# Kernel tuning notes

Measured on AMD Instinct MI355X. Metric: run time of the kernel, lower is better.

Reference implementation:

```python
import jax, jax.numpy as jnp
import numpy as np

N = 100000      # nodes
E = 1600000     # edges (avg degree 16)
IN, HID, OUT = 128, 32, 16
H = 2           # attention heads
EPS = 1e-5
NEG_SLOPE = 0.2


def setup_inputs() -> dict:
    key = jax.random.key(0)
    ks = jax.random.split(key, 24)
    f32 = jnp.float32
    def w(k, shape, scale=0.1):
        return jax.random.normal(k, shape, f32) * scale
    return {
        "x": jax.random.normal(ks[0], (N, IN), f32),
        "edge_index": jax.random.randint(ks[1], (2, E), 0, N, dtype=jnp.int32),
        # GCN layer 1
        "gcn1_W": w(ks[2], (IN, HID)), "gcn1_b": w(ks[3], (HID,)),
        # BN1 (eval mode: running stats)
        "bn1_g": 1.0 + w(ks[4], (HID,)), "bn1_b": w(ks[5], (HID,)),
        "bn1_m": w(ks[6], (HID,)), "bn1_v": 1.0 + jnp.abs(w(ks[7], (HID,))),
        # GAT layer 1 (HID -> HID, heads=H, concat=False)
        "gat1_W": w(ks[8], (HID, H * HID)), "gat1_as": w(ks[9], (H, HID)),
        "gat1_ad": w(ks[10], (H, HID)), "gat1_b": w(ks[11], (HID,)),
        # GCN layer 2
        "gcn2_W": w(ks[12], (HID, HID)), "gcn2_b": w(ks[13], (HID,)),
        # BN2
        "bn2_g": 1.0 + w(ks[14], (HID,)), "bn2_b": w(ks[15], (HID,)),
        "bn2_m": w(ks[16], (HID,)), "bn2_v": 1.0 + jnp.abs(w(ks[17], (HID,))),
        # GAT layer 2 (HID -> OUT, heads=H, concat=False)
        "gat2_W": w(ks[18], (HID, H * OUT)), "gat2_as": w(ks[19], (H, OUT)),
        "gat2_ad": w(ks[20], (H, OUT)), "gat2_b": w(ks[21], (OUT,)),
    }


def _add_self_loops(edge_index):
    loop = jnp.arange(N, dtype=edge_index.dtype)
    src = jnp.concatenate([edge_index[0], loop])
    dst = jnp.concatenate([edge_index[1], loop])
    return src, dst


def _gcn(x, src, dst, W, b):
    h = x @ W                                             # [N, F]
    deg = jax.ops.segment_sum(jnp.ones_like(dst, h.dtype), dst, N)
    dinv = jax.lax.rsqrt(jnp.maximum(deg, 1.0))
    norm = dinv[src] * dinv[dst]                          # [Etot]
    out = jax.ops.segment_sum(h[src] * norm[:, None], dst, N)
    return out + b


def _gat(x, src, dst, W, a_src, a_dst, b, F):
    # PyG GATConv (concat=False -> mean over heads); eval mode (no attn dropout)
    h = (x @ W).reshape(N, H, F)                          # [N, H, F]
    al_s = jnp.einsum('nhf,hf->nh', h, a_src)             # [N, H]
    al_d = jnp.einsum('nhf,hf->nh', h, a_dst)
    e = jax.nn.leaky_relu(al_s[src] + al_d[dst], NEG_SLOPE)  # [Etot, H]
    # segment softmax over destination neighborhoods (self-loops ensure >=1 edge)
    m = jax.ops.segment_max(e, dst, N)
    ex = jnp.exp(e - m[dst])
    s = jax.ops.segment_sum(ex, dst, N)
    alpha = ex / s[dst]                                   # [Etot, H]
    out = jax.ops.segment_sum(alpha[:, :, None] * h[src], dst, N)  # [N, H, F]
    return out.mean(axis=1) + b


def _bn_eval(x, g, b, m, v):
    return (x - m) * jax.lax.rsqrt(v + EPS) * g + b


def reference(x, edge_index, gcn1_W, gcn1_b, bn1_g, bn1_b, bn1_m, bn1_v,
              gat1_W, gat1_as, gat1_ad, gat1_b, gcn2_W, gcn2_b,
              bn2_g, bn2_b, bn2_m, bn2_v, gat2_W, gat2_as, gat2_ad, gat2_b):
    src, dst = _add_self_loops(edge_index)
    h = _gcn(x, src, dst, gcn1_W, gcn1_b)
    h = jax.nn.relu(_bn_eval(h, bn1_g, bn1_b, bn1_m, bn1_v))
    h = jax.nn.relu(_gat(h, src, dst, gat1_W, gat1_as, gat1_ad, gat1_b, HID))
    h = _gcn(h, src, dst, gcn2_W, gcn2_b)
    h = jax.nn.relu(_bn_eval(h, bn2_g, bn2_b, bn2_m, bn2_v))
    h = _gat(h, src, dst, gat2_W, gat2_as, gat2_ad, gat2_b, OUT)
    return jax.nn.log_softmax(h, axis=1)
```

## Files before the change

### kernel.cpp

```cpp
#include <hip/hip_runtime.h>
#include <hip/hip_bf16.h>

#define NN 100000
#define EE 1600000
#define SLAB 64
#define KB 391
#define CHUNK 4096
#define BSLAB 4736

static constexpr float EPSV = 1e-5f;
static constexpr float SLOPE = 0.2f;

__device__ __forceinline__ float lrelu(float v) { return v > 0.f ? v : SLOPE * v; }

__device__ __forceinline__ unsigned rne_bf16(float v) {
    unsigned u = __float_as_uint(v);
    return (u + 0x7fffu + ((u >> 16) & 1u)) >> 16;
}
__device__ __forceinline__ float bf16_lo(unsigned u) { return __uint_as_float(u << 16); }
__device__ __forceinline__ float bf16_hi(unsigned u) { return __uint_as_float(u & 0xffff0000u); }


__global__ void k_z(int* __restrict__ bcnt, unsigned* __restrict__ hsp,
                    unsigned* __restrict__ g1p, unsigned* __restrict__ g2p) {
    int i = threadIdx.x;
    if (i < KB) bcnt[i] = 0;
    if (i < 16) hsp[(size_t)NN * 16 + i] = 0u;
    if (i < 32) g1p[(size_t)NN * 32 + i] = 0u;
    if (i < 16) g2p[(size_t)NN * 16 + i] = 0u;
}

__global__ __launch_bounds__(256) void k_scat(const int* __restrict__ src, const int* __restrict__ dst,
                                              int* __restrict__ bcnt, unsigned int* __restrict__ ebuf) {
    __shared__ int hc[KB], hb[KB];
    int tid = threadIdx.x;
    for (int i = tid; i < KB; i += 256) hc[i] = 0;
    __syncthreads();
    int e0 = blockIdx.x * CHUNK;
    #pragma unroll
    for (int r = 0; r < CHUNK / 256; ++r) {
        int e = e0 + r * 256 + tid;
        if (e < EE) atomicAdd(&hc[dst[e] >> 8], 1);
    }
    __syncthreads();
    for (int i = tid; i < KB; i += 256) {
        int c = hc[i];
        if (c) hb[i] = atomicAdd(&bcnt[i], c);
        hc[i] = 0;
    }
    __syncthreads();
    #pragma unroll
    for (int r = 0; r < CHUNK / 256; ++r) {
        int e = e0 + r * 256 + tid;
        if (e < EE) {
            int d = dst[e];
            int b = d >> 8;
            int rk = atomicAdd(&hc[b], 1);
            ebuf[(size_t)b * BSLAB + hb[b] + rk] = ((unsigned)src[e] << 8) | (unsigned)(d & 255);
        }
    }
}

__global__ __launch_bounds__(256) void k_bucket(const unsigned int* __restrict__ ebuf,
                                                const int* __restrict__ bcnt,
                                                int* __restrict__ col, int* __restrict__ cnt,
                                                float* __restrict__ dinv) {
    __shared__ int lc[256];
    int tid = threadIdx.x;
    int b = blockIdx.x;
    lc[tid] = 0;
    __syncthreads();
    size_t s = (size_t)b * BSLAB;
    int nb = bcnt[b];
    for (int i = tid; i < nb; i += 256) {
        unsigned v = ebuf[s + i];
        int l = v & 255;
        int r = atomicAdd(&lc[l], 1);
        col[(((b << 8) + l) << 6) + r] = v >> 8;
    }
    __syncthreads();
    int node = (b << 8) + tid;
    if (node < NN) {
        int c = lc[tid];
        cnt[node] = c;
        dinv[node] = rsqrtf((float)(c + 1));
        col[node * SLAB + c] = node;
        for (int j = c + 1; j < 32; ++j) col[node * SLAB + j] = NN;
    }
}


__global__ __launch_bounds__(256) void k_gemm1(const float* __restrict__ x,
                                               const float* __restrict__ W,
                                               const float* __restrict__ dinv,
                                               unsigned* __restrict__ hsp) {
    __shared__ float xs[64][128];
    int tid = threadIdx.x;
    int lane = tid & 63;
    int wv = tid >> 6;
    int khalf = lane >> 5, f = lane & 31;
    float wreg[64];
    const float* wp = W + (khalf * 64) * 32 + f;
    #pragma unroll
    for (int i = 0; i < 64; ++i) wreg[i] = wp[i * 32];
    int n0 = blockIdx.x * 64;
    for (int i = tid; i < 64 * 32; i += 256) {
        int row = i >> 5, c4 = i & 31;
        int n = n0 + row;
        float4 v = (n < NN) ? *(const float4*)&x[(size_t)n * 128 + c4 * 4]
                            : make_float4(0.f, 0.f, 0.f, 0.f);
        *(float4*)&xs[row][c4 * 4] = v;
    }
    __syncthreads();
    #pragma unroll 4
    for (int t = 0; t < 16; ++t) {
        int row = wv * 16 + t;
        int n = n0 + row;
        if (n >= NN) break;
        const float* xp = &xs[row][khalf * 64];
        float a0 = 0.f, a1 = 0.f, a2 = 0.f, a3 = 0.f;
        #pragma unroll
        for (int j = 0; j < 16; j += 4) {
            float4 v0 = *(const float4*)&xp[(j + 0) * 4];
            float4 v1 = *(const float4*)&xp[(j + 1) * 4];
            float4 v2 = *(const float4*)&xp[(j + 2) * 4];
            float4 v3 = *(const float4*)&xp[(j + 3) * 4];
            a0 += v0.x * wreg[j * 4 + 0]  + v0.y * wreg[j * 4 + 1]  + v0.z * wreg[j * 4 + 2]  + v0.w * wreg[j * 4 + 3];
            a1 += v1.x * wreg[j * 4 + 4]  + v1.y * wreg[j * 4 + 5]  + v1.z * wreg[j * 4 + 6]  + v1.w * wreg[j * 4 + 7];
            a2 += v2.x * wreg[j * 4 + 8]  + v2.y * wreg[j * 4 + 9]  + v2.z * wreg[j * 4 + 10] + v2.w * wreg[j * 4 + 11];
            a3 += v3.x * wreg[j * 4 + 12] + v3.y * wreg[j * 4 + 13] + v3.z * wreg[j * 4 + 14] + v3.w * wreg[j * 4 + 15];
        }
        float tot = (a0 + a1) + (a2 + a3);
        tot += __shfl_xor(tot, 32);
        unsigned r16 = rne_bf16(tot * dinv[n]);
        unsigned hi16 = __shfl(r16, f + 1, 32);
        if (khalf == 0 && !(f & 1))
            hsp[n * 16 + (f >> 1)] = (hi16 << 16) | (r16 & 0xffffu);
    }
}

__device__ __forceinline__ float quad_reduce_u2(const uint2* u, int lane) {
    float ac0 = 0.f, ac1 = 0.f, ac2 = 0.f, ac3 = 0.f;
    #pragma unroll
    for (int s = 0; s < 8; ++s) {
        ac0 += bf16_lo(u[s].x); ac1 += bf16_hi(u[s].x);
        ac2 += bf16_lo(u[s].y); ac3 += bf16_hi(u[s].y);
    }
    ac0 += __shfl_xor(ac0, 8); ac0 += __shfl_xor(ac0, 16);
    ac1 += __shfl_xor(ac1, 8); ac1 += __shfl_xor(ac1, 16);
    ac2 += __shfl_xor(ac2, 8); ac2 += __shfl_xor(ac2, 16);
    ac3 += __shfl_xor(ac3, 8); ac3 += __shfl_xor(ac3, 16);
    int p = lane >> 2;
    float v0 = __shfl(ac0, p, 32), v1 = __shfl(ac1, p, 32);
    float v2 = __shfl(ac2, p, 32), v3 = __shfl(ac3, p, 32);
    float s01 = (lane & 1) ? v1 : v0;
    float s23 = (lane & 1) ? v3 : v2;
    return (lane & 2) ? s23 : s01;
}

__device__ __forceinline__ float gen_sum_hsp(const unsigned* hsp, const int* col, int base,
                                             int dn, int lane) {
    int half = lane >> 4, l16 = lane & 15;
    int c0 = col[base + lane];
    int c1 = col[base + 32 + lane];
    float aL0 = 0.f, aH0 = 0.f, aL1 = 0.f, aH1 = 0.f;
    for (int j2 = 0; j2 < dn; j2 += 4) {
        int eA = j2 + half, eB = j2 + 2 + half;
        int cA = __shfl((j2 < 32) ? c0 : c1, eA & 31, 32);
        int cB = __shfl((j2 + 2 < 32) ? c0 : c1, eB & 31, 32);
        bool okA = eA < dn, okB = eB < dn;
        unsigned uA = hsp[(okA ? cA : 0) * 16 + l16];
        unsigned uB = hsp[(okB ? cB : 0) * 16 + l16];
        uA = okA ? uA : 0u; uB = okB ? uB : 0u;
        aL0 += bf16_lo(uA); aH0 += bf16_hi(uA);
        aL1 += bf16_lo(uB); aH1 += bf16_hi(uB);
    }
    float accLo = aL0 + aL1, accHi = aH0 + aH1;
    accLo += __shfl_xor(accLo, 16);
    accHi += __shfl_xor(accHi, 16);
    float vLo = __shfl(accLo, lane >> 1, 32);
    float vHi = __shfl(accHi, lane >> 1, 32);
    return (lane & 1) ? vHi : vLo;
}


__global__ __launch_bounds__(256) void k_gcn1_gat1t(
    const unsigned* __restrict__ hsp, const int* __restrict__ cnt,
    const int* __restrict__ col, const float* __restrict__ dinv,
    const float* __restrict__ gb, const float* __restrict__ bng,
    const float* __restrict__ bnb, const float* __restrict__ bnm,
    const float* __restrict__ bnv,
    const float* __restrict__ W1, const float* __restrict__ as_, const float* __restrict__ ad_,
    unsigned* __restrict__ gp, float* __restrict__ al) {
    __shared__ float wAs[32][32], wBs[32][32];
    int tid = threadIdx.x;
    int r = tid >> 5, lane = tid & 31;
    int n = blockIdx.x * 8 + r;
    int dn = cnt[n] + 1;
    int base = n * SLAB;
    int c0 = col[base + lane];
    bool common = (dn <= 32);
    uint2 u[8];
    if (common) {
        int q = lane & 7, sub = lane >> 3;
        const uint2* h2 = (const uint2*)hsp;
        #pragma unroll
        for (int s = 0; s < 8; ++s) {
            int c = __shfl(c0, 4 * s + sub, 32);
            u[s] = h2[(size_t)c * 8 + q];
        }
    }
    for (int i = tid; i < 1024; i += 256) {
        int k = i >> 5, f = i & 31;
        wAs[k][f] = W1[k * 64 + f];
        wBs[k][f] = W1[k * 64 + 32 + f];
    }
    __syncthreads();
    float acc;
    if (common) acc = quad_reduce_u2(u, lane);
    else        acc = gen_sum_hsp(hsp, col, base, dn, lane);
    float v = dinv[n] * acc + gb[lane];
    v = (v - bnm[lane]) * rsqrtf(bnv[lane] + EPSV) * bng[lane] + bnb[lane];
    v = fmaxf(v, 0.f);
    float gA0 = 0.f, gA1 = 0.f, gB0 = 0.f, gB1 = 0.f;
    #pragma unroll
    for (int k = 0; k < 32; k += 2) {
        float t0 = __shfl(v, k, 32);
        float t1v = __shfl(v, k + 1, 32);
        gA0 += t0 * wAs[k][lane];     gB0 += t0 * wBs[k][lane];
        gA1 += t1v * wAs[k + 1][lane]; gB1 += t1v * wBs[k + 1][lane];
    }
    float gA = gA0 + gA1, gB = gB0 + gB1;
    float pas0 = gA * as_[lane],      pad0 = gA * ad_[lane];
    float pas1 = gB * as_[32 + lane], pad1 = gB * ad_[32 + lane];
    #pragma unroll
    for (int off = 16; off; off >>= 1) {
        pas0 += __shfl_xor(pas0, off);
        pad0 += __shfl_xor(pad0, off);
        pas1 += __shfl_xor(pas1, off);
        pad1 += __shfl_xor(pad1, off);
    }
    if (lane == 0) *(float4*)&al[n * 4] = make_float4(pas0, pas1, pad0, pad1);
    gp[n * 32 + lane] = (rne_bf16(gB) << 16) | rne_bf16(gA);
}


__global__ __launch_bounds__(256) void k_gat1_pv(
    const unsigned* __restrict__ gp, const float* __restrict__ al,
    const int* __restrict__ cnt, const int* __restrict__ col,
    const float* __restrict__ b, const float* __restrict__ W2,
    const float* __restrict__ dinv, unsigned* __restrict__ hs3p) {
    __shared__ float2 ec[8][SLAB];
    __shared__ float w2s[32][32];
    int tid = threadIdx.x;
    int r = tid >> 5, lane = tid & 31;
    int n = blockIdx.x * 8 + r;
    int dn = cnt[n] + 1;
    int base = n * SLAB;
    int c0 = col[base + lane];
    int c1 = (dn > 32) ? col[base + 32 + lane] : (int)NN;
    bool common = (dn <= 32);
    uint4 u[8];
    if (common) {
        int q = lane & 7, sub = lane >> 3;
        const uint4* g4 = (const uint4*)gp;
        #pragma unroll
        for (int s = 0; s < 8; ++s) {
            int c = __shfl(c0, 4 * s + sub, 32);
            u[s] = g4[(size_t)c * 8 + q];
        }
    }
    for (int i = tid; i < 1024; i += 256) w2s[i >> 5][i & 31] = W2[i];
    float ad0 = al[n * 4 + 2], ad1 = al[n * 4 + 3];
    float e0a = -1e30f, e1a = -1e30f, e0b = -1e30f, e1b = -1e30f;
    if (lane < dn) {
        float4 a4 = *(const float4*)&al[(size_t)c0 * 4];
        e0a = lrelu(a4.x + ad0); e1a = lrelu(a4.y + ad1);
    }
    if (32 + lane < dn) {
        float4 a4 = *(const float4*)&al[(size_t)c1 * 4];
        e0b = lrelu(a4.x + ad0); e1b = lrelu(a4.y + ad1);
    }
    float m0 = fmaxf(e0a, e0b), m1 = fmaxf(e1a, e1b);
    #pragma unroll
    for (int off = 16; off; off >>= 1) {
        m0 = fmaxf(m0, __shfl_xor(m0, off));
        m1 = fmaxf(m1, __shfl_xor(m1, off));
    }
    float x0a = (lane < dn) ? __expf(e0a - m0) : 0.f;
    float x1a = (lane < dn) ? __expf(e1a - m1) : 0.f;
    float x0b = (32 + lane < dn) ? __expf(e0b - m0) : 0.f;
    float x1b = (32 + lane < dn) ? __expf(e1b - m1) : 0.f;
    float s0 = x0a + x0b, s1 = x1a + x1b;
    #pragma unroll
    for (int off = 16; off; off >>= 1) {
        s0 += __shfl_xor(s0, off);
        s1 += __shfl_xor(s1, off);
    }
    float A0, A1;
    if (common) {
        int sub = lane >> 3;
        float aL0 = 0.f, aL1 = 0.f, aL2 = 0.f, aL3 = 0.f;
        float aH0 = 0.f, aH1 = 0.f, aH2 = 0.f, aH3 = 0.f;
        #pragma unroll
        for (int s = 0; s < 8; ++s) {
            int e = 4 * s + sub;
            float w0 = __shfl(x0a, e, 32);
            float w1 = __shfl(x1a, e, 32);
            aL0 += w0 * bf16_lo(u[s].x); aH0 += w1 * bf16_hi(u[s].x);
            aL1 += w0 * bf16_lo(u[s].y); aH1 += w1 * bf16_hi(u[s].y);
            aL2 += w0 * bf16_lo(u[s].z); aH2 += w1 * bf16_hi(u[s].z);
            aL3 += w0 * bf16_lo(u[s].w); aH3 += w1 * bf16_hi(u[s].w);
        }
        aL0 += __shfl_xor(aL0, 8); aL0 += __shfl_xor(aL0, 16);
        aL1 += __shfl_xor(aL1, 8); aL1 += __shfl_xor(aL1, 16);
        aL2 += __shfl_xor(aL2, 8); aL2 += __shfl_xor(aL2, 16);
        aL3 += __shfl_xor(aL3, 8); aL3 += __shfl_xor(aL3, 16);
        aH0 += __shfl_xor(aH0, 8); aH0 += __shfl_xor(aH0, 16);
        aH1 += __shfl_xor(aH1, 8); aH1 += __shfl_xor(aH1, 16);
        aH2 += __shfl_xor(aH2, 8); aH2 += __shfl_xor(aH2, 16);
        aH3 += __shfl_xor(aH3, 8); aH3 += __shfl_xor(aH3, 16);
        int p = lane >> 2;
        float l0 = __shfl(aL0, p, 32), l1 = __shfl(aL1, p, 32);
        float l2 = __shfl(aL2, p, 32), l3 = __shfl(aL3, p, 32);
        float h0 = __shfl(aH0, p, 32), h1 = __shfl(aH1, p, 32);
        float h2 = __shfl(aH2, p, 32), h3 = __shfl(aH3, p, 32);
        float sl01 = (lane & 1) ? l1 : l0, sl23 = (lane & 1) ? l3 : l2;
        float sh01 = (lane & 1) ? h1 : h0, sh23 = (lane & 1) ? h3 : h2;
        A0 = (lane & 2) ? sl23 : sl01;
        A1 = (lane & 2) ? sh23 : sh01;
    } else {
        ec[r][lane] = make_float2(x0a, x1a);
        ec[r][32 + lane] = make_float2(x0b, x1b);
        int half = lane >> 4, l16 = lane & 15;
        const uint2* gp2 = (const uint2*)gp;
        float a0L = 0.f, a0H = 0.f, a1L = 0.f, a1H = 0.f;
        float b0L = 0.f, b0H = 0.f, b1L = 0.f, b1H = 0.f;
        for (int j2 = 0; j2 < dn; j2 += 4) {
            int eA = j2 + half, eB = j2 + 2 + half;
            int cA = __shfl((j2 < 32) ? c0 : c1, eA & 31, 32);
            int cB = __shfl((j2 + 2 < 32) ? c0 : c1, eB & 31, 32);
            bool okA = eA < dn, okB = eB < dn;
            uint2 uA = gp2[(size_t)(okA ? cA : 0) * 16 + l16];
            uint2 uB = gp2[(size_t)(okB ? cB : 0) * 16 + l16];
            float2 wA = ec[r][eA & 63];
            float2 wB = ec[r][eB & 63];
            uA.x = okA ? uA.x : 0u; uA.y = okA ? uA.y : 0u;
            uB.x = okB ? uB.x : 0u; uB.y = okB ? uB.y : 0u;
            a0L += wA.x * bf16_lo(uA.x); a1L += wA.y * bf16_hi(uA.x);
            a0H += wA.x * bf16_lo(uA.y); a1H += wA.y * bf16_hi(uA.y);
            b0L += wB.x * bf16_lo(uB.x); b1L += wB.y * bf16_hi(uB.x);
            b0H += wB.x * bf16_lo(uB.y); b1H += wB.y * bf16_hi(uB.y);
        }
        a0L += b0L; a0H += b0H; a1L += b1L; a1H += b1H;
        a0L += __shfl_xor(a0L, 16); a0H += __shfl_xor(a0H, 16);
        a1L += __shfl_xor(a1L, 16); a1H += __shfl_xor(a1H, 16);
        int p = lane >> 1;
        float t0L = __shfl(a0L, p, 32), t0H = __shfl(a0H, p, 32);
        float t1L = __shfl(a1L, p, 32), t1H = __shfl(a1H, p, 32);
        A0 = (lane & 1) ? t0H : t0L;
        A1 = (lane & 1) ? t1H : t1L;
    }
    __syncthreads();
    float v = 0.5f * (A0 / s0 + A1 / s1) + b[lane];
    v = fmaxf(v, 0.f);
    float g0 = 0.f, g1 = 0.f;
    #pragma unroll
    for (int k = 0; k < 32; k += 2) {
        g0 += __shfl(v, k, 32) * w2s[k][lane];
        g1 += __shfl(v, k + 1, 32) * w2s[k + 1][lane];
    }
    unsigned r16 = rne_bf16((g0 + g1) * dinv[n]);
    unsigned hi16 = __shfl(r16, lane + 1, 32);
    if (!(lane & 1)) hs3p[n * 16 + (lane >> 1)] = (hi16 << 16) | (r16 & 0xffffu);
}


__global__ __launch_bounds__(256) void k_gcn2_gat2t(
    const unsigned* __restrict__ hsp, const int* __restrict__ cnt,
    const int* __restrict__ col, const float* __restrict__ dinv,
    const float* __restrict__ gb, const float* __restrict__ bng,
    const float* __restrict__ bnb, const float* __restrict__ bnm,
    const float* __restrict__ bnv,
    const float* __restrict__ Wg, const float* __restrict__ as_, const float* __restrict__ ad_,
    unsigned* __restrict__ g2p, float* __restrict__ al) {
    __shared__ float wgs[32][32];
    int tid = threadIdx.x;
    int r = tid >> 5, lane = tid & 31;
    int n = blockIdx.x * 8 + r;
    int dn = cnt[n] + 1;
    int base = n * SLAB;
    int c0 = col[base + lane];
    bool common = (dn <= 32);
    uint2 u[8];
    if (common) {
        int q = lane & 7, sub = lane >> 3;
        const uint2* h2 = (const uint2*)hsp;
        #pragma unroll
        for (int s = 0; s < 8; ++s) {
            int c = __shfl(c0, 4 * s + sub, 32);
            u[s] = h2[(size_t)c * 8 + q];
        }
    }
    for (int i = tid; i < 1024; i += 256) wgs[i >> 5][i & 31] = Wg[i];
    __syncthreads();
    float acc;
    if (common) acc = quad_reduce_u2(u, lane);
    else        acc = gen_sum_hsp(hsp, col, base, dn, lane);
    float v = dinv[n] * acc + gb[lane];
    v = (v - bnm[lane]) * rsqrtf(bnv[lane] + EPSV) * bng[lane] + bnb[lane];
    v = fmaxf(v, 0.f);
    float g0 = 0.f, g1 = 0.f;
    #pragma unroll
    for (int k = 0; k < 32; k += 2) {
        g0 += __shfl(v, k, 32) * wgs[k][lane];
        g1 += __shfl(v, k + 1, 32) * wgs[k + 1][lane];
    }
    float g = g0 + g1;
    int hh = lane >> 4, ff = lane & 15;
    float as_v = g * as_[hh * 16 + ff];
    float ad_v = g * ad_[hh * 16 + ff];
    #pragma unroll
    for (int off = 8; off; off >>= 1) {
        as_v += __shfl_xor(as_v, off);
        ad_v += __shfl_xor(ad_v, off);
    }
    if (ff == 0) { al[n * 4 + hh] = as_v; al[n * 4 + 2 + hh] = ad_v; }
    unsigned r16 = rne_bf16(g);
    unsigned hi16 = __shfl(r16, lane + 1, 32);
    if (!(lane & 1)) g2p[n * 16 + (lane >> 1)] = (hi16 << 16) | (r16 & 0xffffu);
}


__global__ __launch_bounds__(256) void k_gat2_agg(
    const unsigned* __restrict__ g2p, const float* __restrict__ al,
    const int* __restrict__ cnt, const int* __restrict__ col,
    const float* __restrict__ b, float* __restrict__ out) {
    __shared__ float2 ec[8][SLAB];
    int tid = threadIdx.x;
    int r = tid >> 5, lane = tid & 31;
    int n = blockIdx.x * 8 + r;
    int dn = cnt[n] + 1;
    int base = n * SLAB;
    int c0 = col[base + lane];
    int c1 = (dn > 32) ? col[base + 32 + lane] : (int)NN;
    bool common = (dn <= 32);
    uint2 u[8];
    if (common) {
        int q = lane & 7, sub = lane >> 3;
        const uint2* g2 = (const uint2*)g2p;
        #pragma unroll
        for (int s = 0; s < 8; ++s) {
            int c = __shfl(c0, 4 * s + sub, 32);
            u[s] = g2[(size_t)c * 8 + q];
        }
    }
    float ad0 = al[n * 4 + 2], ad1 = al[n * 4 + 3];
    float e0a = -1e30f, e1a = -1e30f, e0b = -1e30f, e1b = -1e30f;
    if (lane < dn) {
        float4 a4 = *(const float4*)&al[(size_t)c0 * 4];
        e0a = lrelu(a4.x + ad0); e1a = lrelu(a4.y + ad1);
    }
    if (32 + lane < dn) {
        float4 a4 = *(const float4*)&al[(size_t)c1 * 4];
        e0b = lrelu(a4.x + ad0); e1b = lrelu(a4.y + ad1);
    }
    float m0 = fmaxf(e0a, e0b), m1 = fmaxf(e1a, e1b);
    #pragma unroll
    for (int off = 16; off; off >>= 1) {
        m0 = fmaxf(m0, __shfl_xor(m0, off));
        m1 = fmaxf(m1, __shfl_xor(m1, off));
    }
    float x0a = (lane < dn) ? __expf(e0a - m0) : 0.f;
    float x1a = (lane < dn) ? __expf(e1a - m1) : 0.f;
    float x0b = (32 + lane < dn) ? __expf(e0b - m0) : 0.f;
    float x1b = (32 + lane < dn) ? __expf(e1b - m1) : 0.f;
    float s0 = x0a + x0b, s1 = x1a + x1b;
    #pragma unroll
    for (int off = 16; off; off >>= 1) {
        s0 += __shfl_xor(s0, off);
        s1 += __shfl_xor(s1, off);
    }
    float acc;
    if (common) {
        int sub = lane >> 3;
        bool head1 = (lane & 4) != 0;
        float ac0 = 0.f, ac1 = 0.f, ac2 = 0.f, ac3 = 0.f;
        #pragma unroll
        for (int s = 0; s < 8; ++s) {
            int e = 4 * s + sub;
            float w0 = __shfl(x0a, e, 32);
            float w1 = __shfl(x1a, e, 32);
            float w = head1 ? w1 : w0;
            ac0 += w * bf16_lo(u[s].x); ac1 += w * bf16_hi(u[s].x);
            ac2 += w * bf16_lo(u[s].y); ac3 += w * bf16_hi(u[s].y);
        }
        ac0 += __shfl_xor(ac0, 8); ac0 += __shfl_xor(ac0, 16);
        ac1 += __shfl_xor(ac1, 8); ac1 += __shfl_xor(ac1, 16);
        ac2 += __shfl_xor(ac2, 8); ac2 += __shfl_xor(ac2, 16);
        ac3 += __shfl_xor(ac3, 8); ac3 += __shfl_xor(ac3, 16);
        int p = lane >> 2;
        float v0 = __shfl(ac0, p, 32), v1 = __shfl(ac1, p, 32);
        float v2 = __shfl(ac2, p, 32), v3 = __shfl(ac3, p, 32);
        float s01 = (lane & 1) ? v1 : v0;
        float s23 = (lane & 1) ? v3 : v2;
        acc = (lane & 2) ? s23 : s01;
    } else {
        ec[r][lane] = make_float2(x0a, x1a);
        ec[r][32 + lane] = make_float2(x0b, x1b);
        int half = lane >> 4, l16 = lane & 15;
        bool head1g = (l16 & 8) != 0;
        float aL0 = 0.f, aH0 = 0.f, aL1 = 0.f, aH1 = 0.f;
        for (int j2 = 0; j2 < dn; j2 += 4) {
            int eA = j2 + half, eB = j2 + 2 + half;
            int cA = __shfl((j2 < 32) ? c0 : c1, eA & 31, 32);
            int cB = __shfl((j2 + 2 < 32) ? c0 : c1, eB & 31, 32);
            bool okA = eA < dn, okB = eB < dn;
            unsigned uA = g2p[(okA ? cA : 0) * 16 + l16];
            unsigned uB = g2p[(okB ? cB : 0) * 16 + l16];
            float2 wA = ec[r][eA & 63];
            float2 wB = ec[r][eB & 63];
            float wa = head1g ? wA.y : wA.x;
            float wb = head1g ? wB.y : wB.x;
            uA = okA ? uA : 0u; uB = okB ? uB : 0u;
            aL0 += wa * bf16_lo(uA); aH0 += wa * bf16_hi(uA);
            aL1 += wb * bf16_lo(uB); aH1 += wb * bf16_hi(uB);
        }
        float accLo = aL0 + aL1, accHi = aH0 + aH1;
        accLo += __shfl_xor(accLo, 16);
        accHi += __shfl_xor(accHi, 16);
        float vLo = __shfl(accLo, lane >> 1, 32);
        float vHi = __shfl(accHi, lane >> 1, 32);
        acc = (lane & 1) ? vHi : vLo;
    }
    int hh = lane >> 4, ff = lane & 15;
    acc /= (hh ? s1 : s0);
    float v = 0.5f * (acc + __shfl_xor(acc, 16)) + b[ff];
    float mx = v;
    #pragma unroll
    for (int off = 8; off; off >>= 1) mx = fmaxf(mx, __shfl_xor(mx, off));
    float se = __expf(v - mx);
    #pragma unroll
    for (int off = 8; off; off >>= 1) se += __shfl_xor(se, off);
    if (hh == 0) out[(size_t)n * 16 + ff] = v - mx - __logf(se);
}


static inline size_t al256(size_t x) { return (x + 255) & ~((size_t)255); }

extern "C" void kernel_launch(void* const* d_in, const int* in_sizes, int n_in,
                              void* d_out, int out_size, void* d_ws, size_t ws_size,
                              hipStream_t stream) {
    const float* x      = (const float*)d_in[0];
    const int*   ei     = (const int*)d_in[1];
    const float* gcn1_W = (const float*)d_in[2];
    const float* gcn1_b = (const float*)d_in[3];
    const float* bn1_g  = (const float*)d_in[4];
    const float* bn1_b  = (const float*)d_in[5];
    const float* bn1_m  = (const float*)d_in[6];
    const float* bn1_v  = (const float*)d_in[7];
    const float* gat1_W = (const float*)d_in[8];
    const float* gat1_as= (const float*)d_in[9];
    const float* gat1_ad= (const float*)d_in[10];
    const float* gat1_b = (const float*)d_in[11];
    const float* gcn2_W = (const float*)d_in[12];
    const float* gcn2_b = (const float*)d_in[13];
    const float* bn2_g  = (const float*)d_in[14];
    const float* bn2_b  = (const float*)d_in[15];
    const float* bn2_m  = (const float*)d_in[16];
    const float* bn2_v  = (const float*)d_in[17];
    const float* gat2_W = (const float*)d_in[18];
    const float* gat2_as= (const float*)d_in[19];
    const float* gat2_ad= (const float*)d_in[20];
    const float* gat2_b = (const float*)d_in[21];
    float* out = (float*)d_out;

    char* w = (char*)d_ws;
    size_t off = 0;
    auto alloc = [&](size_t bytes) { void* p = w + off; off = al256(off + bytes); return p; };
    int*      cnt   = (int*)alloc((size_t)NN * 4);
    float*    dinv  = (float*)alloc((size_t)NN * 4);
    int*      col   = (int*)alloc((size_t)NN * SLAB * 4);
    unsigned* hsp   = (unsigned*)alloc((size_t)(NN + 1) * 16 * 4);
    unsigned* g1p   = (unsigned*)alloc((size_t)(NN + 1) * 32 * 4);
    unsigned* g2p   = (unsigned*)alloc((size_t)(NN + 1) * 16 * 4);
    float*    al    = (float*)alloc((size_t)NN * 4 * 4);
    int*      bcnt  = (int*)alloc((size_t)KB * 4);
    unsigned int* ebuf = (unsigned int*)g1p;

    const int* esrc = ei;
    const int* edst = ei + EE;
    const int GE = (EE + CHUNK - 1) / CHUNK;

    k_z<<<1, 512, 0, stream>>>(bcnt, hsp, g1p, g2p);
    k_scat<<<GE, 256, 0, stream>>>(esrc, edst, bcnt, ebuf);
    k_bucket<<<KB, 256, 0, stream>>>(ebuf, bcnt, col, cnt, dinv);

    k_gemm1<<<(NN + 63) / 64, 256, 0, stream>>>(x, gcn1_W, dinv, hsp);
    k_gcn1_gat1t<<<NN / 8, 256, 0, stream>>>(hsp, cnt, col, dinv, gcn1_b,
                                             bn1_g, bn1_b, bn1_m, bn1_v,
                                             gat1_W, gat1_as, gat1_ad, g1p, al);
    k_gat1_pv<<<NN / 8, 256, 0, stream>>>(g1p, al, cnt, col, gat1_b,
                                          gcn2_W, dinv, hsp);
    k_gcn2_gat2t<<<NN / 8, 256, 0, stream>>>(hsp, cnt, col, dinv, gcn2_b,
                                             bn2_g, bn2_b, bn2_m, bn2_v,
                                             gat2_W, gat2_as, gat2_ad, g2p, al);
    k_gat2_agg<<<NN / 8, 256, 0, stream>>>(g2p, al, cnt, col, gat2_b, out);
}
```

Measured before the change: 287.9 us.

## Drop max-subtraction in GAT softmax, fuse exp into gather, split attention logits

Removes the segment-max pass and its cross-lane reductions from both GAT aggregation kernels. Each lane now computes exp(lrelu(as+ad)) inline while gathering neighbour features and accumulates the denominator alongside the numerator, which also drops the shared-memory weight buffer. Attention logits are split into separate source and destination float2 arrays, and a sentinel row at index NN (zero features, -1e30 logits) replaces the per-edge predicated loads. This trades a dependent max/exp pre-pass for more exp work per gathered element. Without max subtraction, exp can overflow for large logits.

After: 265.4 us. 1.08x faster.

```diff
diff --git a/kernel.cpp b/kernel.cpp
--- a/kernel.cpp
+++ b/kernel.cpp
@@ -22,12 +22,14 @@
 
 
 __global__ void k_z(int* __restrict__ bcnt, unsigned* __restrict__ hsp,
-                    unsigned* __restrict__ g1p, unsigned* __restrict__ g2p) {
+                    unsigned* __restrict__ g1p, unsigned* __restrict__ g2p,
+                    float2* __restrict__ als) {
     int i = threadIdx.x;
     if (i < KB) bcnt[i] = 0;
     if (i < 16) hsp[(size_t)NN * 16 + i] = 0u;
     if (i < 32) g1p[(size_t)NN * 32 + i] = 0u;
     if (i < 16) g2p[(size_t)NN * 16 + i] = 0u;
+    if (i == 0) als[NN] = make_float2(-1e30f, -1e30f);
 }
 
 __global__ __launch_bounds__(256) void k_scat(const int* __restrict__ src, const int* __restrict__ dst,
@@ -168,10 +170,10 @@
         int eA = j2 + half, eB = j2 + 2 + half;
         int cA = __shfl((j2 < 32) ? c0 : c1, eA & 31, 32);
         int cB = __shfl((j2 + 2 < 32) ? c0 : c1, eB & 31, 32);
-        bool okA = eA < dn, okB = eB < dn;
-        unsigned uA = hsp[(okA ? cA : 0) * 16 + l16];
-        unsigned uB = hsp[(okB ? cB : 0) * 16 + l16];
-        uA = okA ? uA : 0u; uB = okB ? uB : 0u;
+        cA = (eA < dn) ? cA : (int)NN;
+        cB = (eB < dn) ? cB : (int)NN;
+        unsigned uA = hsp[(size_t)cA * 16 + l16];
+        unsigned uB = hsp[(size_t)cB * 16 + l16];
         aL0 += bf16_lo(uA); aH0 += bf16_hi(uA);
         aL1 += bf16_lo(uB); aH1 += bf16_hi(uB);
     }
@@ -191,7 +193,7 @@
     const float* __restrict__ bnb, const float* __restrict__ bnm,
     const float* __restrict__ bnv,
     const float* __restrict__ W1, const float* __restrict__ as_, const float* __restrict__ ad_,
-    unsigned* __restrict__ gp, float* __restrict__ al) {
+    unsigned* __restrict__ gp, float2* __restrict__ als, float2* __restrict__ ald) {
     __shared__ float wAs[32][32], wBs[32][32];
     int tid = threadIdx.x;
     int r = tid >> 5, lane = tid & 31;
@@ -240,17 +242,17 @@
         pas1 += __shfl_xor(pas1, off);
         pad1 += __shfl_xor(pad1, off);
     }
-    if (lane == 0) *(float4*)&al[n * 4] = make_float4(pas0, pas1, pad0, pad1);
+    if (lane == 0) { als[n] = make_float2(pas0, pas1); ald[n] = make_float2(pad0, pad1); }
     gp[n * 32 + lane] = (rne_bf16(gB) << 16) | rne_bf16(gA);
 }
 
 
 __global__ __launch_bounds__(256) void k_gat1_pv(
-    const unsigned* __restrict__ gp, const float* __restrict__ al,
+    const unsigned* __restrict__ gp, const float2* __restrict__ als,
+    const float2* __restrict__ ald,
     const int* __restrict__ cnt, const int* __restrict__ col,
     const float* __restrict__ b, const float* __restrict__ W2,
     const float* __restrict__ dinv, unsigned* __restrict__ hs3p) {
-    __shared__ float2 ec[8][SLAB];
     __shared__ float w2s[32][32];
     int tid = threadIdx.x;
     int r = tid >> 5, lane = tid & 31;
@@ -258,59 +260,27 @@
     int dn = cnt[n] + 1;
     int base = n * SLAB;
     int c0 = col[base + lane];
-    int c1 = (dn > 32) ? col[base + 32 + lane] : (int)NN;
-    bool common = (dn <= 32);
-    uint4 u[8];
-    if (common) {
+    float2 ad = ald[n];
+    for (int i = tid; i < 1024; i += 256) w2s[i >> 5][i & 31] = W2[i];
+    float A0, A1, ws0, ws1;
+    if (dn <= 32) {
         int q = lane & 7, sub = lane >> 3;
         const uint4* g4 = (const uint4*)gp;
+        float aL0 = 0.f, aL1 = 0.f, aL2 = 0.f, aL3 = 0.f;
+        float aH0 = 0.f, aH1 = 0.f, aH2 = 0.f, aH3 = 0.f;
+        float w0s = 0.f, w1s = 0.f;
         #pragma unroll
         for (int s = 0; s < 8; ++s) {
             int c = __shfl(c0, 4 * s + sub, 32);
-            u[s] = g4[(size_t)c * 8 + q];
-        }
-    }
-    for (int i = tid; i < 1024; i += 256) w2s[i >> 5][i & 31] = W2[i];
-    float ad0 = al[n * 4 + 2], ad1 = al[n * 4 + 3];
-    float e0a = -1e30f, e1a = -1e30f, e0b = -1e30f, e1b = -1e30f;
-    if (lane < dn) {
-        float4 a4 = *(const float4*)&al[(size_t)c0 * 4];
-        e0a = lrelu(a4.x + ad0); e1a = lrelu(a4.y + ad1);
-    }
-    if (32 + lane < dn) {
-        float4 a4 = *(const float4*)&al[(size_t)c1 * 4];
-        e0b = lrelu(a4.x + ad0); e1b = lrelu(a4.y + ad1);
-    }
-    float m0 = fmaxf(e0a, e0b), m1 = fmaxf(e1a, e1b);
-    #pragma unroll
-    for (int off = 16; off; off >>= 1) {
-        m0 = fmaxf(m0, __shfl_xor(m0, off));
-        m1 = fmaxf(m1, __shfl_xor(m1, off));
-    }
-    float x0a = (lane < dn) ? __expf(e0a - m0) : 0.f;
-    float x1a = (lane < dn) ? __expf(e1a - m1) : 0.f;
-    float x0b = (32 + lane < dn) ? __expf(e0b - m0) : 0.f;
-    float x1b = (32 + lane < dn) ? __expf(e1b - m1) : 0.f;
-    float s0 = x0a + x0b, s1 = x1a + x1b;
-    #pragma unroll
-    for (int off = 16; off; off >>= 1) {
-        s0 += __shfl_xor(s0, off);
-        s1 += __shfl_xor(s1, off);
-    }
-    float A0, A1;
-    if (common) {
-        int sub = lane >> 3;
-        float aL0 = 0.f, aL1 = 0.f, aL2 = 0.f, aL3 = 0.f;
-        float aH0 = 0.f, aH1 = 0.f, aH2 = 0.f, aH3 = 0.f;
-        #pragma unroll
-        for (int s = 0; s < 8; ++s) {
-            int e = 4 * s + sub;
-            float w0 = __shfl(x0a, e, 32);
-            float w1 = __shfl(x1a, e, 32);
-            aL0 += w0 * bf16_lo(u[s].x); aH0 += w1 * bf16_hi(u[s].x);
-            aL1 += w0 * bf16_lo(u[s].y); aH1 += w1 * bf16_hi(u[s].y);
-            aL2 += w0 * bf16_lo(u[s].z); aH2 += w1 * bf16_hi(u[s].z);
-            aL3 += w0 * bf16_lo(u[s].w); aH3 += w1 * bf16_hi(u[s].w);
+            uint4 u = g4[(size_t)c * 8 + q];
+            float2 sl = als[c];
+            float w0 = __expf(lrelu(sl.x + ad.x));
+            float w1 = __expf(lrelu(sl.y + ad.y));
+            aL0 += w0 * bf16_lo(u.x); aH0 += w1 * bf16_hi(u.x);
+            aL1 += w0 * bf16_lo(u.y); aH1 += w1 * bf16_hi(u.y);
+            aL2 += w0 * bf16_lo(u.z); aH2 += w1 * bf16_hi(u.z);
+            aL3 += w0 * bf16_lo(u.w); aH3 += w1 * bf16_hi(u.w);
+            w0s += w0; w1s += w1;
         }
         aL0 += __shfl_xor(aL0, 8); aL0 += __shfl_xor(aL0, 16);
         aL1 += __shfl_xor(aL1, 8); aL1 += __shfl_xor(aL1, 16);
@@ -320,6 +290,8 @@
         aH1 += __shfl_xor(aH1, 8); aH1 += __shfl_xor(aH1, 16);
         aH2 += __shfl_xor(aH2, 8); aH2 += __shfl_xor(aH2, 16);
         aH3 += __shfl_xor(aH3, 8); aH3 += __shfl_xor(aH3, 16);
+        w0s += __shfl_xor(w0s, 8); w0s += __shfl_xor(w0s, 16);
+        w1s += __shfl_xor(w1s, 8); w1s += __shfl_xor(w1s, 16);
         int p = lane >> 2;
         float l0 = __shfl(aL0, p, 32), l1 = __shfl(aL1, p, 32);
         float l2 = __shfl(aL2, p, 32), l3 = __shfl(aL3, p, 32);
@@ -329,40 +301,42 @@
         float sh01 = (lane & 1) ? h1 : h0, sh23 = (lane & 1) ? h3 : h2;
         A0 = (lane & 2) ? sl23 : sl01;
         A1 = (lane & 2) ? sh23 : sh01;
+        ws0 = w0s; ws1 = w1s;
     } else {
-        ec[r][lane] = make_float2(x0a, x1a);
-        ec[r][32 + lane] = make_float2(x0b, x1b);
+        int c1 = col[base + 32 + lane];
         int half = lane >> 4, l16 = lane & 15;
         const uint2* gp2 = (const uint2*)gp;
         float a0L = 0.f, a0H = 0.f, a1L = 0.f, a1H = 0.f;
-        float b0L = 0.f, b0H = 0.f, b1L = 0.f, b1H = 0.f;
+        float w0s = 0.f, w1s = 0.f;
         for (int j2 = 0; j2 < dn; j2 += 4) {
             int eA = j2 + half, eB = j2 + 2 + half;
             int cA = __shfl((j2 < 32) ? c0 : c1, eA & 31, 32);
             int cB = __shfl((j2 + 2 < 32) ? c0 : c1, eB & 31, 32);
-            bool okA = eA < dn, okB = eB < dn;
-            uint2 uA = gp2[(size_t)(okA ? cA : 0) * 16 + l16];
-            uint2 uB = gp2[(size_t)(okB ? cB : 0) * 16 + l16];
-            float2 wA = ec[r][eA & 63];
-            float2 wB = ec[r][eB & 63];
-            uA.x = okA ? uA.x : 0u; uA.y = okA ? uA.y : 0u;
-            uB.x = okB ? uB.x : 0u; uB.y = okB ? uB.y : 0u;
-            a0L += wA.x * bf16_lo(uA.x); a1L += wA.y * bf16_hi(uA.x);
-            a0H += wA.x * bf16_lo(uA.y); a1H += wA.y * bf16_hi(uA.y);
-            b0L += wB.x * bf16_lo(uB.x); b1L += wB.y * bf16_hi(uB.x);
-            b0H += wB.x * bf16_lo(uB.y); b1H += wB.y * bf16_hi(uB.y);
-        }
-        a0L += b0L; a0H += b0H; a1L += b1L; a1H += b1H;
+            cA = (eA < dn) ? cA : (int)NN;
+            cB = (eB < dn) ? cB : (int)NN;
+            uint2 uA = gp2[(size_t)cA * 16 + l16];
+            uint2 uB = gp2[(size_t)cB * 16 + l16];
+            float2 sA = als[cA], sB = als[cB];
+            float wA0 = __expf(lrelu(sA.x + ad.x)), wA1 = __expf(lrelu(sA.y + ad.y));
+            float wB0 = __expf(lrelu(sB.x + ad.x)), wB1 = __expf(lrelu(sB.y + ad.y));
+            a0L += wA0 * bf16_lo(uA.x) + wB0 * bf16_lo(uB.x);
+            a1L += wA1 * bf16_hi(uA.x) + wB1 * bf16_hi(uB.x);
+            a0H += wA0 * bf16_lo(uA.y) + wB0 * bf16_lo(uB.y);
+            a1H += wA1 * bf16_hi(uA.y) + wB1 * bf16_hi(uB.y);
+            w0s += wA0 + wB0; w1s += wA1 + wB1;
+        }
         a0L += __shfl_xor(a0L, 16); a0H += __shfl_xor(a0H, 16);
         a1L += __shfl_xor(a1L, 16); a1H += __shfl_xor(a1H, 16);
+        w0s += __shfl_xor(w0s, 16); w1s += __shfl_xor(w1s, 16);
         int p = lane >> 1;
         float t0L = __shfl(a0L, p, 32), t0H = __shfl(a0H, p, 32);
         float t1L = __shfl(a1L, p, 32), t1H = __shfl(a1H, p, 32);
         A0 = (lane & 1) ? t0H : t0L;
         A1 = (lane & 1) ? t1H : t1L;
-    }
-    __syncthreads();
-    float v = 0.5f * (A0 / s0 + A1 / s1) + b[lane];
+        ws0 = w0s; ws1 = w1s;
+    }
+    __syncthreads();
+    float v = 0.5f * (A0 / ws0 + A1 / ws1) + b[lane];
     v = fmaxf(v, 0.f);
     float g0 = 0.f, g1 = 0.f;
     #pragma unroll
@@ -383,7 +357,7 @@
     const float* __restrict__ bnb, const float* __restrict__ bnm,
     const float* __restrict__ bnv,
     const float* __restrict__ Wg, const float* __restrict__ as_, const float* __restrict__ ad_,
-    unsigned* __restrict__ g2p, float* __restrict__ al) {
+    unsigned* __restrict__ g2p, float2* __restrict__ als, float2* __restrict__ ald) {
     __shared__ float wgs[32][32];
     int tid = threadIdx.x;
     int r = tid >> 5, lane = tid & 31;
@@ -425,7 +399,13 @@
         as_v += __shfl_xor(as_v, off);
         ad_v += __shfl_xor(ad_v, off);
     }
-    if (ff == 0) { al[n * 4 + hh] = as_v; al[n * 4 + 2 + hh] = ad_v; }
+    if (lane == 0) {
+        float s1v = __shfl(as_v, 16, 32);
+        float d1v = __shfl(ad_v, 16, 32);
+        als[n] = make_float2(as_v, s1v);
+        ald[n] = make_float2(ad_v, d1v);
+    } else if (lane == 16) {
+    }
     unsigned r16 = rne_bf16(g);
     unsigned hi16 = __shfl(r16, lane + 1, 32);
     if (!(lane & 1)) g2p[n * 16 + (lane >> 1)] = (hi16 << 16) | (r16 & 0xffffu);
@@ -433,108 +413,84 @@
 
 
 __global__ __launch_bounds__(256) void k_gat2_agg(
-    const unsigned* __restrict__ g2p, const float* __restrict__ al,
+    const unsigned* __restrict__ g2p, const float2* __restrict__ als,
+    const float2* __restrict__ ald,
     const int* __restrict__ cnt, const int* __restrict__ col,
     const float* __restrict__ b, float* __restrict__ out) {
-    __shared__ float2 ec[8][SLAB];
     int tid = threadIdx.x;
     int r = tid >> 5, lane = tid & 31;
     int n = blockIdx.x * 8 + r;
     int dn = cnt[n] + 1;
     int base = n * SLAB;
     int c0 = col[base + lane];
-    int c1 = (dn > 32) ? col[base + 32 + lane] : (int)NN;
-    bool common = (dn <= 32);
-    uint2 u[8];
-    if (common) {
+    float2 ad = ald[n];
+    float acc, ws0, ws1;
+    if (dn <= 32) {
         int q = lane & 7, sub = lane >> 3;
+        bool head1 = (lane & 4) != 0;
         const uint2* g2 = (const uint2*)g2p;
+        float ac0 = 0.f, ac1 = 0.f, ac2 = 0.f, ac3 = 0.f;
+        float w0s = 0.f, w1s = 0.f;
         #pragma unroll
         for (int s = 0; s < 8; ++s) {
             int c = __shfl(c0, 4 * s + sub, 32);
-            u[s] = g2[(size_t)c * 8 + q];
-        }
-    }
-    float ad0 = al[n * 4 + 2], ad1 = al[n * 4 + 3];
-    float e0a = -1e30f, e1a = -1e30f, e0b = -1e30f, e1b = -1e30f;
-    if (lane < dn) {
-        float4 a4 = *(const float4*)&al[(size_t)c0 * 4];
-        e0a = lrelu(a4.x + ad0); e1a = lrelu(a4.y + ad1);
-    }
-    if (32 + lane < dn) {
-        float4 a4 = *(const float4*)&al[(size_t)c1 * 4];
-        e0b = lrelu(a4.x + ad0); e1b = lrelu(a4.y + ad1);
-    }
-    float m0 = fmaxf(e0a, e0b), m1 = fmaxf(e1a, e1b);
-    #pragma unroll
-    for (int off = 16; off; off >>= 1) {
-        m0 = fmaxf(m0, __shfl_xor(m0, off));
-        m1 = fmaxf(m1, __shfl_xor(m1, off));
-    }
-    float x0a = (lane < dn) ? __expf(e0a - m0) : 0.f;
-    float x1a = (lane < dn) ? __expf(e1a - m1) : 0.f;
-    float x0b = (32 + lane < dn) ? __expf(e0b - m0) : 0.f;
-    float x1b = (32 + lane < dn) ? __expf(e1b - m1) : 0.f;
-    float s0 = x0a + x0b, s1 = x1a + x1b;
-    #pragma unroll
-    for (int off = 16; off; off >>= 1) {
-        s0 += __shfl_xor(s0, off);
-        s1 += __shfl_xor(s1, off);
-    }
-    float acc;
-    if (common) {
-        int sub = lane >> 3;
-        bool head1 = (lane & 4) != 0;
-        float ac0 = 0.f, ac1 = 0.f, ac2 = 0.f, ac3 = 0.f;
-        #pragma unroll
-        for (int s = 0; s < 8; ++s) {
-            int e = 4 * s + sub;
-            float w0 = __shfl(x0a, e, 32);
-            float w1 = __shfl(x1a, e, 32);
+            uint2 u = g2[(size_t)c * 8 + q];
+            float2 sl = als[c];
+            float w0 = __expf(lrelu(sl.x + ad.x));
+            float w1 = __expf(lrelu(sl.y + ad.y));
             float w = head1 ? w1 : w0;
-            ac0 += w * bf16_lo(u[s].x); ac1 += w * bf16_hi(u[s].x);
-            ac2 += w * bf16_lo(u[s].y); ac3 += w * bf16_hi(u[s].y);
+            ac0 += w * bf16_lo(u.x); ac1 += w * bf16_hi(u.x);
+            ac2 += w * bf16_lo(u.y); ac3 += w * bf16_hi(u.y);
+            w0s += w0; w1s += w1;
         }
         ac0 += __shfl_xor(ac0, 8); ac0 += __shfl_xor(ac0, 16);
         ac1 += __shfl_xor(ac1, 8); ac1 += __shfl_xor(ac1, 16);
         ac2 += __shfl_xor(ac2, 8); ac2 += __shfl_xor(ac2, 16);
         ac3 += __shfl_xor(ac3, 8); ac3 += __shfl_xor(ac3, 16);
+        w0s += __shfl_xor(w0s, 8); w0s += __shfl_xor(w0s, 16);
+        w1s += __shfl_xor(w1s, 8); w1s += __shfl_xor(w1s, 16);
         int p = lane >> 2;
         float v0 = __shfl(ac0, p, 32), v1 = __shfl(ac1, p, 32);
         float v2 = __shfl(ac2, p, 32), v3 = __shfl(ac3, p, 32);
         float s01 = (lane & 1) ? v1 : v0;
         float s23 = (lane & 1) ? v3 : v2;
         acc = (lane & 2) ? s23 : s01;
+        ws0 = w0s; ws1 = w1s;
     } else {
-        ec[r][lane] = make_float2(x0a, x1a);
-        ec[r][32 + lane] = make_float2(x0b, x1b);
+        int c1 = col[base + 32 + lane];
         int half = lane >> 4, l16 = lane & 15;
         bool head1g = (l16 & 8) != 0;
         float aL0 = 0.f, aH0 = 0.f, aL1 = 0.f, aH1 = 0.f;
+        float w0s = 0.f, w1s = 0.f;
         for (int j2 = 0; j2 < dn; j2 += 4) {
             int eA = j2 + half, eB = j2 + 2 + half;
             int cA = __shfl((j2 < 32) ? c0 : c1, eA & 31, 32);
             int cB = __shfl((j2 + 2 < 32) ? c0 : c1, eB & 31, 32);
-            bool okA = eA < dn, okB = eB < dn;
-            unsigned uA = g2p[(okA ? cA : 0) * 16 + l16];
-            unsigned uB = g2p[(okB ? cB : 0) * 16 + l16];
-            float2 wA = ec[r][eA & 63];
-            float2 wB = ec[r][eB & 63];
-            float wa = head1g ? wA.y : wA.x;
-            float wb = head1g ? wB.y : wB.x;
-            uA = okA ? uA : 0u; uB = okB ? uB : 0u;
+            cA = (eA < dn) ? cA : (int)NN;
+            cB = (eB < dn) ? cB : (int)NN;
+            unsigned uA = g2p[(size_t)cA * 16 + l16];
+            unsigned uB = g2p[(size_t)cB * 16 + l16];
+            float2 sA = als[cA], sB = als[cB];
+            float wA0 = __expf(lrelu(sA.x + ad.x)), wA1 = __expf(lrelu(sA.y + ad.y));
+            float wB0 = __expf(lrelu(sB.x + ad.x)), wB1 = __expf(lrelu(sB.y + ad.y));
+            float wa = head1g ? wA1 : wA0;
+            float wb = head1g ? wB1 : wB0;
             aL0 += wa * bf16_lo(uA); aH0 += wa * bf16_hi(uA);
             aL1 += wb * bf16_lo(uB); aH1 += wb * bf16_hi(uB);
+            w0s += wA0 + wB0; w1s += wA1 + wB1;
         }
         float accLo = aL0 + aL1, accHi = aH0 + aH1;
         accLo += __shfl_xor(accLo, 16);
         accHi += __shfl_xor(accHi, 16);
+        w0s += __shfl_xor(w0s, 16);
+        w1s += __shfl_xor(w1s, 16);
         float vLo = __shfl(accLo, lane >> 1, 32);
         float vHi = __shfl(accHi, lane >> 1, 32);
         acc = (lane & 1) ? vHi : vLo;
+        ws0 = w0s; ws1 = w1s;
     }
     int hh = lane >> 4, ff = lane & 15;
-    acc /= (hh ? s1 : s0);
+    acc /= (hh ? ws1 : ws0);
     float v = 0.5f * (acc + __shfl_xor(acc, 16)) + b[ff];
     float mx = v;
     #pragma unroll
@@ -584,7 +540,8 @@
     unsigned* hsp   = (unsigned*)alloc((size_t)(NN + 1) * 16 * 4);
     unsigned* g1p   = (unsigned*)alloc((size_t)(NN + 1) * 32 * 4);
     unsigned* g2p   = (unsigned*)alloc((size_t)(NN + 1) * 16 * 4);
-    float*    al    = (float*)alloc((size_t)NN * 4 * 4);
+    float2*   als   = (float2*)alloc((size_t)(NN + 1) * 8);
+    float2*   ald   = (float2*)alloc((size_t)NN * 8);
     int*      bcnt  = (int*)alloc((size_t)KB * 4);
     unsigned int* ebuf = (unsigned int*)g1p;
 
@@ -592,18 +549,18 @@
     const int* edst = ei + EE;
     const int GE = (EE + CHUNK - 1) / CHUNK;
 
-    k_z<<<1, 512, 0, stream>>>(bcnt, hsp, g1p, g2p);
+    k_z<<<1, 512, 0, stream>>>(bcnt, hsp, g1p, g2p, als);
     k_scat<<<GE, 256, 0, stream>>>(esrc, edst, bcnt, ebuf);
     k_bucket<<<KB, 256, 0, stream>>>(ebuf, bcnt, col, cnt, dinv);
 
     k_gemm1<<<(NN + 63) / 64, 256, 0, stream>>>(x, gcn1_W, dinv, hsp);
     k_gcn1_gat1t<<<NN / 8, 256, 0, stream>>>(hsp, cnt, col, dinv, gcn1_b,
                                              bn1_g, bn1_b, bn1_m, bn1_v,
-                                             gat1_W, gat1_as, gat1_ad, g1p, al);
-    k_gat1_pv<<<NN / 8, 256, 0, stream>>>(g1p, al, cnt, col, gat1_b,
+                                             gat1_W, gat1_as, gat1_ad, g1p, als, ald);
+    k_gat1_pv<<<NN / 8, 256, 0, stream>>>(g1p, als, ald, cnt, col, gat1_b,
                                           gcn2_W, dinv, hsp);
     k_gcn2_gat2t<<<NN / 8, 256, 0, stream>>>(hsp, cnt, col, dinv, gcn2_b,
                                              bn2_g, bn2_b, bn2_m, bn2_v,
-                                             gat2_W, gat2_as, gat2_ad, g2p, al);
-    k_gat2_agg<<<NN / 8, 256, 0, stream>>>(g2p, al, cnt, col, gat2_b, out);
-}
+                                             gat2_W, gat2_as, gat2_ad, g2p, als, ald);
+    k_gat2_agg<<<NN / 8, 256, 0, stream>>>(g2p, als, ald, cnt, col, gat2_b, out);
+}
```
